# Performance work log

Measured on AMD Instinct MI355X. Metric: run time of the kernel, lower is better.

Reference implementation:

```python
import jax, jax.numpy as jnp
import numpy as np

D_MODEL = 1024
NUM_HEADS = 16
HEAD_DIM = 64
INNER = NUM_HEADS * HEAD_DIM


def setup_inputs() -> dict:
    key = jax.random.key(0)
    k_x, k_q, k_k, k_v, k_o = jax.random.split(key, 5)
    B, T = 4, 2048
    s = 1.0 / np.sqrt(D_MODEL)
    return {
        "x": jax.random.normal(k_x, (B, T, D_MODEL), dtype=jnp.float32),
        "W_q": jax.random.uniform(k_q, (D_MODEL, INNER), dtype=jnp.float32, minval=-s, maxval=s),
        "W_k": jax.random.uniform(k_k, (D_MODEL, INNER), dtype=jnp.float32, minval=-s, maxval=s),
        "W_v": jax.random.uniform(k_v, (D_MODEL, INNER), dtype=jnp.float32, minval=-s, maxval=s),
        "W_o": jax.random.uniform(k_o, (INNER, D_MODEL), dtype=jnp.float32, minval=-s, maxval=s),
    }


def reference(x, W_q, W_k, W_v, W_o):
    B, T, _ = x.shape
    scale = HEAD_DIM ** -0.5
    # project and split heads: [B, H, T, Dh]
    q = (x @ W_q).reshape(B, T, NUM_HEADS, HEAD_DIM).transpose(0, 2, 1, 3)
    k = (x @ W_k).reshape(B, T, NUM_HEADS, HEAD_DIM).transpose(0, 2, 1, 3)
    v = (x @ W_v).reshape(B, T, NUM_HEADS, HEAD_DIM).transpose(0, 2, 1, 3)
    scores = jnp.einsum("bhqd,bhkd->bhqk", q, k) * scale  # [B,H,T,T]
    causal = jnp.tril(jnp.ones((T, T), dtype=bool))
    scores = jnp.where(causal, scores, -jnp.inf)
    probs = jax.nn.softmax(scores, axis=-1)
    ctx = jnp.einsum("bhqk,bhkd->bhqd", probs, v)
    ctx = ctx.transpose(0, 2, 1, 3).reshape(B, T, INNER)
    return ctx @ W_o
```

## Files before the change

### kernel.cpp

```cpp
#include <hip/hip_runtime.h>


typedef short  short8  __attribute__((ext_vector_type(8)));
typedef short  short4v __attribute__((ext_vector_type(4)));
typedef float  floatx4 __attribute__((ext_vector_type(4)));
typedef unsigned uint2v __attribute__((ext_vector_type(2)));

#define T_SZ 2048
#define DM   1024

#define QSCALE 0.18033688011112042f

__device__ __forceinline__ short f2bf(float f) {
  unsigned u = __float_as_uint(f);
  u += 0x7fffu + ((u >> 16) & 1u);
  return (short)(u >> 16);
}

#if defined(__has_builtin) && __has_builtin(__builtin_amdgcn_cvt_pk_bf16_f32)
typedef __bf16 bf16x2_t __attribute__((ext_vector_type(2)));
__device__ __forceinline__ unsigned pack_bf(float lo, float hi) {
  return __builtin_bit_cast(unsigned, __builtin_amdgcn_cvt_pk_bf16_f32(lo, hi));
}
#else
__device__ __forceinline__ unsigned pack_bf(float lo, float hi) {
  return __builtin_amdgcn_perm(__float_as_uint(hi) + 0x8000u,
                               __float_as_uint(lo) + 0x8000u, 0x07060302u);
}
#endif

#if defined(__has_builtin) && __has_builtin(__builtin_amdgcn_exp2f)
__device__ __forceinline__ float fexp2(float x) { return __builtin_amdgcn_exp2f(x); }
#else
__device__ __forceinline__ float fexp2(float x) { return exp2f(x); }
#endif

__device__ __forceinline__ void gll16(const void* g, void* l) {
  __builtin_amdgcn_global_load_lds((const __attribute__((address_space(1))) void*)g,
                                   (__attribute__((address_space(3))) void*)l, 16, 0, 0);
}

#define SBAR() asm volatile("s_barrier" ::: "memory")
#define WLG()  asm volatile("s_waitcnt lgkmcnt(0)" ::: "memory")
#define WV6()  asm volatile("s_waitcnt vmcnt(6)" ::: "memory")
#define WV0()  asm volatile("s_waitcnt vmcnt(0)" ::: "memory")

__global__ void cvt_kernel(const float* __restrict__ s0, const float* __restrict__ s1,
                           const float* __restrict__ s2, const float* __restrict__ s3,
                           short* __restrict__ dst,
                           const float* __restrict__ x, short* __restrict__ xb) {
  const int tx = threadIdx.x, ty = threadIdx.y;
  if (blockIdx.z == 4) {
    const int tid = ty * 32 + tx;
    const int blk = blockIdx.y * 32 + blockIdx.x;
    int i = (blk * 256 + tid) * 4;
#pragma unroll
    for (int j = 0; j < 8; ++j) {
      const float4 v = *(const float4*)(x + i);
      short4v o;
      o.x = f2bf(v.x); o.y = f2bf(v.y); o.z = f2bf(v.z); o.w = f2bf(v.w);
      *(short4v*)(xb + i) = o;
      i += 1048576;
    }
    return;
  }
  const float* srcs[4] = {s0, s1, s2, s3};
  const float* src = srcs[blockIdx.z];
  short* d = dst + (size_t)blockIdx.z * 1048576;
  __shared__ float tile[32][33];
  const int n_base = blockIdx.x * 32, k_base = blockIdx.y * 32;
#pragma unroll
  for (int j = 0; j < 4; ++j)
    tile[ty + j * 8][tx] = src[(size_t)(k_base + ty + j * 8) * 1024 + n_base + tx];
  __syncthreads();
#pragma unroll
  for (int j = 0; j < 4; ++j)
    d[(size_t)(n_base + ty + j * 8) * 1024 + k_base + tx] = f2bf(tile[tx][ty + j * 8]);
}

template <int MODE>
__global__ __launch_bounds__(512, 2) void gemm8(
    const short* __restrict__ A, const short* __restrict__ B,
    short* __restrict__ obf, short* __restrict__ vt, float* __restrict__ of) {
  __shared__ short As[2 * 128 * 64];
  __shared__ short Bs[2 * 256 * 64];
  const int tid  = threadIdx.x;
  const int w    = tid >> 6, lane = tid & 63;
  const int quad = lane >> 4, l15 = lane & 15;
  const int wr   = w >> 2, wc = w & 3;
  const int fx   = l15 & 7;
  const int lid  = (int)blockIdx.x;
  const int xcd  = lid & 7, idx = lid >> 3;
  const int m0   = (idx >> 2) * 128;
  const int n0   = (xcd * 4 + (idx & 3)) * 256;
  const int srow = tid >> 3;
  const int scol = ((tid & 7) ^ (srow & 7)) * 8;

  const short* Ag = A + (size_t)(m0 + srow) * 1024 + scol;
  const short* Bg = B + (size_t)(n0 + srow) * 1024 + scol;

  floatx4 acc[4][4] = {};
  short8 af[4][2], bf[4][2];

#define STG_A(slot, kb) do { \
    short* _lb = &As[(slot) * 8192 + tid * 8]; \
    const short* _gp = Ag + (kb); \
    gll16(_gp, _lb); \
    gll16(_gp + (size_t)(64 * 1024), _lb + 4096); \
  } while (0)
#define STG_B(slot, kb) do { \
    short* _lb = &Bs[(slot) * 16384 + tid * 8]; \
    const short* _gp = Bg + (kb); \
    gll16(_gp,                         _lb); \
    gll16(_gp + (size_t)( 64 * 1024), _lb + 4096); \
    gll16(_gp + (size_t)(128 * 1024), _lb + 8192); \
    gll16(_gp + (size_t)(192 * 1024), _lb + 12288); \
  } while (0)
#define LDA_ALL(slot) do { \
    _Pragma("unroll") for (int ii = 0; ii < 4; ++ii) \
    _Pragma("unroll") for (int s = 0; s < 2; ++s) \
      af[ii][s] = *(const short8*)&As[(slot) * 8192 + \
          (wr * 64 + ii * 16 + l15) * 64 + ((s * 4 + quad) ^ fx) * 8]; \
  } while (0)
#define LDB_ALL(slot) do { \
    _Pragma("unroll") for (int j = 0; j < 4; ++j) \
    _Pragma("unroll") for (int s = 0; s < 2; ++s) \
      bf[j][s] = *(const short8*)&Bs[(slot) * 16384 + \
          (wc * 64 + j * 16 + l15) * 64 + ((s * 4 + quad) ^ fx) * 8]; \
  } while (0)
#define MMH(ih) do { \
    __builtin_amdgcn_s_setprio(1); \
    _Pragma("unroll") for (int i2 = 0; i2 < 2; ++i2) \
    _Pragma("unroll") for (int j = 0; j < 4; ++j) \
    _Pragma("unroll") for (int s = 0; s < 2; ++s) \
      acc[(ih) * 2 + i2][j] = __builtin_amdgcn_mfma_f32_16x16x32_bf16( \
          af[(ih) * 2 + i2][s], bf[j][s], acc[(ih) * 2 + i2][j], 0, 0, 0); \
    __builtin_amdgcn_s_setprio(0); \
  } while (0)

  STG_B(0, 0);  STG_A(0, 0);
  STG_B(1, 64); STG_A(1, 64);
  WV6(); SBAR();

  for (int t = 0; t < 8; ++t) {
    const int kn2 = (2 * t + 2) * 64;
    const int kn3 = (2 * t + 3) * 64;
    const bool mre = (t < 7);
    LDA_ALL(0); LDB_ALL(0);
    SBAR(); WLG();
    MMH(0);
    SBAR();
    if (mre) STG_B(0, kn2);
    if (mre) STG_A(0, kn2);
    MMH(1);
    if (mre) WV6(); else WV0();
    SBAR();
    LDA_ALL(1); LDB_ALL(1);
    SBAR(); WLG();
    MMH(0);
    SBAR();
    if (mre) STG_B(1, kn3);
    if (mre) STG_A(1, kn3);
    MMH(1);
    if (mre) WV6();
    SBAR();
  }

  if constexpr (MODE == 0) {
    const int wsel = m0 >> 10;
    const int nn0  = (m0 & 1023) + wr * 64;
    if (wsel < 2) {
      const float scale = (wsel == 0) ? QSCALE : 1.0f;
      short* outw = obf + (size_t)wsel * (64u * 2048u * 64u);
#pragma unroll
      for (int i = 0; i < 4; ++i) {
        const int nn = nn0 + i * 16 + quad * 4;
        const int h = nn >> 6, d = nn & 63;
#pragma unroll
        for (int j = 0; j < 4; ++j) {
          const int tg = n0 + wc * 64 + j * 16 + l15;
          const int b = tg >> 11, tt = tg & 2047;
          short4v o4;
#pragma unroll
          for (int r = 0; r < 4; ++r) o4[r] = f2bf(acc[i][j][r] * scale);
          *(short4v*)(outw + (((size_t)(b * 16 + h) * 2048 + tt) << 6) + d) = o4;
        }
      }
    } else {
#pragma unroll
      for (int i = 0; i < 4; ++i) {
        const int nn = nn0 + i * 16 + quad * 4;
        const int h = nn >> 6, d = nn & 63;
#pragma unroll
        for (int j = 0; j < 4; ++j) {
          const int tg = n0 + wc * 64 + j * 16 + l15;
          const int b = tg >> 11, tt = tg & 2047;
#pragma unroll
          for (int r = 0; r < 4; ++r)
            vt[(((size_t)(b * 16 + h) * 64 + d + r) << 11) + tt] = f2bf(acc[i][j][r]);
        }
      }
    }
  } else {
    const int nn0 = m0 + wr * 64;
#pragma unroll
    for (int i = 0; i < 4; ++i) {
      const int nn = nn0 + i * 16 + quad * 4;
#pragma unroll
      for (int j = 0; j < 4; ++j) {
        const int tg = n0 + wc * 64 + j * 16 + l15;
        float4 o4;
        o4.x = acc[i][j][0]; o4.y = acc[i][j][1];
        o4.z = acc[i][j][2]; o4.w = acc[i][j][3];
        *(float4*)(of + (size_t)tg * 1024 + nn) = o4;
      }
    }
  }
#undef STG_A
#undef STG_B
#undef LDA_ALL
#undef LDB_ALL
#undef MMH
}

__global__ __launch_bounds__(512, 4) void attn_kernel(
    const short* __restrict__ Qg, const short* __restrict__ Kg,
    const short* __restrict__ Vt, short* __restrict__ ctx) {
  __shared__ short Ks[128 * 72];
  __shared__ short Vs[80 * 136];
  __shared__ short Ps[8 * 32 * 40];

  const int tid  = threadIdx.x;
  const int w    = tid >> 6, lane = tid & 63;
  const int quad = lane >> 4, l15 = lane & 15;
  const int bh = (int)blockIdx.x + 8 * ((int)blockIdx.y & 7);
  const int g  = (int)blockIdx.y >> 3;
  const int qb = (g < 4) ? (7 - g) : (g - 4);
  const int b  = bh >> 4, h = bh & 15;

  const size_t base = (size_t)bh * (T_SZ * 64);
  const short* Qb  = Qg + base;
  const short* Kb  = Kg + base;
  const short* Vtb = Vt + base;
  short* Pw = &Ps[w * 1280];

  const int skr = tid >> 2, skp = (tid & 3) * 16;
  const int svr = tid >> 3, svp = (tid & 7) * 16;

  if (tid < 256) {
    const int rr = 64 + (tid >> 4), cb = (tid & 15) * 8;
    const short vv = (tid < 16) ? (short)0x3F80 : (short)0;
    short8 fill;
#pragma unroll
    for (int j = 0; j < 8; ++j) fill[j] = vv;
    *(short8*)&Vs[rr * 136 + cb] = fill;
  }

  const int rowA = qb * 256 + w * 32;
  const int rowB = rowA + 16;
  const int ktmax = 2 * qb + 2;

  const short8 qA0 = *(const short8*)(Qb + (size_t)(rowA + l15) * 64 + quad * 8);
  const short8 qA1 = *(const short8*)(Qb + (size_t)(rowA + l15) * 64 + 32 + quad * 8);
  const short8 qB0 = *(const short8*)(Qb + (size_t)(rowB + l15) * 64 + quad * 8);
  const short8 qB1 = *(const short8*)(Qb + (size_t)(rowB + l15) * 64 + 32 + quad * 8);

  floatx4 OA[4] = {}, OB[4] = {};
  floatx4 O5A = {}, O5B = {};

  short8 kR[2], vR[2];
  kR[0] = *(const short8*)(Kb + (size_t)skr * 64 + skp);
  kR[1] = *(const short8*)(Kb + (size_t)skr * 64 + skp + 8);
  vR[0] = *(const short8*)(Vtb + (size_t)svr * 2048 + svp);
  vR[1] = *(const short8*)(Vtb + (size_t)svr * 2048 + svp + 8);

  for (int kt = 0; kt < ktmax; ++kt) {
    const int k0 = kt << 7;
    __syncthreads();
    *(short8*)&Ks[skr * 72 + skp]     = kR[0];
    *(short8*)&Ks[skr * 72 + skp + 8] = kR[1];
    *(short8*)&Vs[svr * 136 + svp]     = vR[0];
    *(short8*)&Vs[svr * 136 + svp + 8] = vR[1];
    if (kt + 1 < ktmax) {
      const int kn = (kt + 1) << 7;
      kR[0] = *(const short8*)(Kb + (size_t)(kn + skr) * 64 + skp);
      kR[1] = *(const short8*)(Kb + (size_t)(kn + skr) * 64 + skp + 8);
      vR[0] = *(const short8*)(Vtb + (size_t)svr * 2048 + kn + svp);
      vR[1] = *(const short8*)(Vtb + (size_t)svr * 2048 + kn + svp + 8);
    }
    __syncthreads();

    const int dkA = rowA - k0;
    if (dkA < 0) continue;
    const int dkB = dkA + 16;
    const int limA = dkA + l15, limB = limA + 16;
    const int naA = min(8, (dkA >> 4) + 1), nchA = (naA + 1) >> 1;
    const int naB = min(8, (dkB >> 4) + 1), nchB = (naB + 1) >> 1;

#pragma unroll
    for (int c = 0; c < 4; ++c) {
      if (c < nchB) {
#pragma unroll
        for (int mm = 0; mm < 2; ++mm) {
          const int mt = 2 * c + mm;
          const int pa = l15 * 40 + mm * 16 + quad * 4;
          const int pb = (16 + l15) * 40 + mm * 16 + quad * 4;
          const bool aB = (mt * 16 < dkB + 16);
          const bool aA = (mt * 16 < dkA + 16);
          if (aB) {
            const short8 kf0 = *(const short8*)&Ks[(mt * 16 + l15) * 72 + quad * 8];
            const short8 kf1 = *(const short8*)&Ks[(mt * 16 + l15) * 72 + 32 + quad * 8];
            {
              floatx4 s = {};
              s = __builtin_amdgcn_mfma_f32_16x16x32_bf16(kf0, qB0, s, 0, 0, 0);
              s = __builtin_amdgcn_mfma_f32_16x16x32_bf16(kf1, qB1, s, 0, 0, 0);
              if (mt * 16 + 15 > dkB) {
#pragma unroll
                for (int r = 0; r < 4; ++r)
                  if (mt * 16 + quad * 4 + r > limB) s[r] = -1e30f;
              }
              floatx4 e;
#pragma unroll
              for (int r = 0; r < 4; ++r) e[r] = fexp2(s[r]);
              uint2v pd;
              pd.x = pack_bf(e[0], e[1]);
              pd.y = pack_bf(e[2], e[3]);
              *(uint2v*)&Pw[pb] = pd;
            }
            if (c < nchA) {
              if (aA) {
                floatx4 s = {};
                s = __builtin_amdgcn_mfma_f32_16x16x32_bf16(kf0, qA0, s, 0, 0, 0);
                s = __builtin_amdgcn_mfma_f32_16x16x32_bf16(kf1, qA1, s, 0, 0, 0);
                if (mt * 16 + 15 > dkA) {
#pragma unroll
                  for (int r = 0; r < 4; ++r)
                    if (mt * 16 + quad * 4 + r > limA) s[r] = -1e30f;
                }
                floatx4 e;
#pragma unroll
                for (int r = 0; r < 4; ++r) e[r] = fexp2(s[r]);
                uint2v pd;
                pd.x = pack_bf(e[0], e[1]);
                pd.y = pack_bf(e[2], e[3]);
                *(uint2v*)&Pw[pa] = pd;
              } else {
                uint2v z; z.x = 0; z.y = 0;
                *(uint2v*)&Pw[pa] = z;
              }
            }
          } else {
            uint2v z; z.x = 0; z.y = 0;
            *(uint2v*)&Pw[pb] = z;
            if (c < nchA) *(uint2v*)&Pw[pa] = z;
          }
        }
        const int vcol = c * 32 + quad * 8;
        const short8 vfl = *(const short8*)&Vs[(64 + l15) * 136 + vcol];
        short8 vf[4];
#pragma unroll
        for (int dt = 0; dt < 4; ++dt)
          vf[dt] = *(const short8*)&Vs[(dt * 16 + l15) * 136 + vcol];
        const short8 pfB = *(const short8*)&Pw[(16 + l15) * 40 + quad * 8];
#pragma unroll
        for (int dt = 0; dt < 4; ++dt)
          OB[dt] = __builtin_amdgcn_mfma_f32_16x16x32_bf16(vf[dt], pfB, OB[dt], 0, 0, 0);
        O5B = __builtin_amdgcn_mfma_f32_16x16x32_bf16(vfl, pfB, O5B, 0, 0, 0);
        if (c < nchA) {
          const short8 pfA = *(const short8*)&Pw[l15 * 40 + quad * 8];
#pragma unroll
          for (int dt = 0; dt < 4; ++dt)
            OA[dt] = __builtin_amdgcn_mfma_f32_16x16x32_bf16(vf[dt], pfA, OA[dt], 0, 0, 0);
          O5A = __builtin_amdgcn_mfma_f32_16x16x32_bf16(vfl, pfA, O5A, 0, 0, 0);
        }
      }
    }
  }

  {
    const float lA = __shfl(O5A[0], l15);
    const float invA = 1.0f / lA;
    const int t = rowA + l15;
    short* cb = ctx + (((size_t)(b * T_SZ + t)) << 10) + h * 64 + quad * 4;
#pragma unroll
    for (int dt = 0; dt < 4; ++dt) {
      short4v o4;
#pragma unroll
      for (int r = 0; r < 4; ++r) o4[r] = f2bf(OA[dt][r] * invA);
      *(short4v*)(cb + dt * 16) = o4;
    }
  }
  {
    const float lB = __shfl(O5B[0], l15);
    const float invB = 1.0f / lB;
    const int t = rowB + l15;
    short* cb = ctx + (((size_t)(b * T_SZ + t)) << 10) + h * 64 + quad * 4;
#pragma unroll
    for (int dt = 0; dt < 4; ++dt) {
      short4v o4;
#pragma unroll
      for (int r = 0; r < 4; ++r) o4[r] = f2bf(OB[dt][r] * invB);
      *(short4v*)(cb + dt * 16) = o4;
    }
  }
}

extern "C" void kernel_launch(void* const* d_in, const int* in_sizes, int n_in,
                              void* d_out, int out_size, void* d_ws, size_t ws_size,
                              hipStream_t stream) {
  const float* x  = (const float*)d_in[0];
  const float* Wq = (const float*)d_in[1];
  const float* Wk = (const float*)d_in[2];
  const float* Wv = (const float*)d_in[3];
  const float* Wo = (const float*)d_in[4];
  float* out = (float*)d_out;

  short* ws  = (short*)d_ws;
  short* xb  = ws;
  short* Wt  = ws + 8388608;
  short* Qb  = Wt + 4 * 1048576;
  short* Kb  = Qb + 8388608;
  short* Vt  = Kb + 8388608;
  short* ctx = xb;

  cvt_kernel<<<dim3(32, 32, 5), dim3(32, 8), 0, stream>>>(Wq, Wk, Wv, Wo, Wt, x, xb);
  gemm8<0><<<dim3(768), 512, 0, stream>>>(Wt, xb, Qb, Vt, nullptr);
  attn_kernel<<<dim3(8, 64), 512, 0, stream>>>(Qb, Kb, Vt, ctx);
  gemm8<1><<<dim3(256), 512, 0, stream>>>(Wt + 3 * 1048576, ctx, nullptr, nullptr, out);
}
```

Baseline: 236.7 us.

## Shrink GEMM tile to 128x128 with 4 waves and finer-grained staging

```diff
diff --git a/kernel.cpp b/kernel.cpp
--- a/kernel.cpp
+++ b/kernel.cpp
@@ -42,7 +42,7 @@
 
 #define SBAR() asm volatile("s_barrier" ::: "memory")
 #define WLG()  asm volatile("s_waitcnt lgkmcnt(0)" ::: "memory")
-#define WV6()  asm volatile("s_waitcnt vmcnt(6)" ::: "memory")
+#define WV8()  asm volatile("s_waitcnt vmcnt(8)" ::: "memory")
 #define WV0()  asm volatile("s_waitcnt vmcnt(0)" ::: "memory")
 
 __global__ void cvt_kernel(const float* __restrict__ s0, const float* __restrict__ s1,
@@ -79,20 +79,20 @@
 }
 
 template <int MODE>
-__global__ __launch_bounds__(512, 2) void gemm8(
+__global__ __launch_bounds__(256, 2) void gemm4(
     const short* __restrict__ A, const short* __restrict__ B,
     short* __restrict__ obf, short* __restrict__ vt, float* __restrict__ of) {
   __shared__ short As[2 * 128 * 64];
-  __shared__ short Bs[2 * 256 * 64];
+  __shared__ short Bs[2 * 128 * 64];
   const int tid  = threadIdx.x;
   const int w    = tid >> 6, lane = tid & 63;
   const int quad = lane >> 4, l15 = lane & 15;
-  const int wr   = w >> 2, wc = w & 3;
+  const int wr   = w >> 1, wc = w & 1;
   const int fx   = l15 & 7;
   const int lid  = (int)blockIdx.x;
   const int xcd  = lid & 7, idx = lid >> 3;
-  const int m0   = (idx >> 2) * 128;
-  const int n0   = (xcd * 4 + (idx & 3)) * 256;
+  const int m0   = (idx >> 3) * 128;
+  const int n0   = (xcd * 8 + (idx & 7)) * 128;
   const int srow = tid >> 3;
   const int scol = ((tid & 7) ^ (srow & 7)) * 8;
 
@@ -100,69 +100,75 @@
   const short* Bg = B + (size_t)(n0 + srow) * 1024 + scol;
 
   floatx4 acc[4][4] = {};
-  short8 af[4][2], bf[4][2];
-
-#define STG_A(slot, kb) do { \
-    short* _lb = &As[(slot) * 8192 + tid * 8]; \
-    const short* _gp = Ag + (kb); \
-    gll16(_gp, _lb); \
-    gll16(_gp + (size_t)(64 * 1024), _lb + 4096); \
-  } while (0)
-#define STG_B(slot, kb) do { \
-    short* _lb = &Bs[(slot) * 16384 + tid * 8]; \
-    const short* _gp = Bg + (kb); \
-    gll16(_gp,                         _lb); \
-    gll16(_gp + (size_t)( 64 * 1024), _lb + 4096); \
-    gll16(_gp + (size_t)(128 * 1024), _lb + 8192); \
-    gll16(_gp + (size_t)(192 * 1024), _lb + 12288); \
-  } while (0)
-#define LDA_ALL(slot) do { \
-    _Pragma("unroll") for (int ii = 0; ii < 4; ++ii) \
+  short8 af[2][2], bf[4][2];
+
+#define SA0(slot, kb) do { \
+    gll16(Ag + (kb),                        &As[(slot) * 8192 + tid * 8]); \
+    gll16(Ag + (size_t)(32 * 1024) + (kb),  &As[(slot) * 8192 + 2048 + tid * 8]); \
+  } while (0)
+#define SA1(slot, kb) do { \
+    gll16(Ag + (size_t)(64 * 1024) + (kb),  &As[(slot) * 8192 + 4096 + tid * 8]); \
+    gll16(Ag + (size_t)(96 * 1024) + (kb),  &As[(slot) * 8192 + 6144 + tid * 8]); \
+  } while (0)
+#define SB0(slot, kb) do { \
+    gll16(Bg + (kb),                        &Bs[(slot) * 8192 + tid * 8]); \
+    gll16(Bg + (size_t)(32 * 1024) + (kb),  &Bs[(slot) * 8192 + 2048 + tid * 8]); \
+  } while (0)
+#define SB1(slot, kb) do { \
+    gll16(Bg + (size_t)(64 * 1024) + (kb),  &Bs[(slot) * 8192 + 4096 + tid * 8]); \
+    gll16(Bg + (size_t)(96 * 1024) + (kb),  &Bs[(slot) * 8192 + 6144 + tid * 8]); \
+  } while (0)
+#define LDA4(slot, ih) do { \
+    _Pragma("unroll") for (int ii = 0; ii < 2; ++ii) \
     _Pragma("unroll") for (int s = 0; s < 2; ++s) \
       af[ii][s] = *(const short8*)&As[(slot) * 8192 + \
-          (wr * 64 + ii * 16 + l15) * 64 + ((s * 4 + quad) ^ fx) * 8]; \
-  } while (0)
-#define LDB_ALL(slot) do { \
+          (wr * 64 + (ih) * 32 + ii * 16 + l15) * 64 + ((s * 4 + quad) ^ fx) * 8]; \
+  } while (0)
+#define LDB8(slot) do { \
     _Pragma("unroll") for (int j = 0; j < 4; ++j) \
     _Pragma("unroll") for (int s = 0; s < 2; ++s) \
-      bf[j][s] = *(const short8*)&Bs[(slot) * 16384 + \
+      bf[j][s] = *(const short8*)&Bs[(slot) * 8192 + \
           (wc * 64 + j * 16 + l15) * 64 + ((s * 4 + quad) ^ fx) * 8]; \
   } while (0)
-#define MMH(ih) do { \
+#define MMQ(ih, jh) do { \
     __builtin_amdgcn_s_setprio(1); \
-    _Pragma("unroll") for (int i2 = 0; i2 < 2; ++i2) \
-    _Pragma("unroll") for (int j = 0; j < 4; ++j) \
+    _Pragma("unroll") for (int ii = 0; ii < 2; ++ii) \
+    _Pragma("unroll") for (int jj = 0; jj < 2; ++jj) \
     _Pragma("unroll") for (int s = 0; s < 2; ++s) \
-      acc[(ih) * 2 + i2][j] = __builtin_amdgcn_mfma_f32_16x16x32_bf16( \
-          af[(ih) * 2 + i2][s], bf[j][s], acc[(ih) * 2 + i2][j], 0, 0, 0); \
+      acc[(ih) * 2 + ii][(jh) * 2 + jj] = __builtin_amdgcn_mfma_f32_16x16x32_bf16( \
+          af[ii][s], bf[(jh) * 2 + jj][s], acc[(ih) * 2 + ii][(jh) * 2 + jj], 0, 0, 0); \
     __builtin_amdgcn_s_setprio(0); \
   } while (0)
 
-  STG_B(0, 0);  STG_A(0, 0);
-  STG_B(1, 64); STG_A(1, 64);
-  WV6(); SBAR();
+  SB0(0, 0);  SB1(0, 0);  SA0(0, 0);  SA1(0, 0);
+  SB0(1, 64); SB1(1, 64); SA0(1, 64); SA1(1, 64);
+  WV8(); SBAR();
 
   for (int t = 0; t < 8; ++t) {
     const int kn2 = (2 * t + 2) * 64;
     const int kn3 = (2 * t + 3) * 64;
     const bool mre = (t < 7);
-    LDA_ALL(0); LDB_ALL(0);
-    SBAR(); WLG();
-    MMH(0);
+    LDA4(0, 0); LDB8(0);
+    SBAR(); WLG(); MMQ(0, 0); SBAR();
+    if (mre) SB0(0, kn2);
+    MMQ(0, 1); SBAR();
+    LDA4(0, 1);
+    if (mre) SB1(0, kn2);
+    SBAR(); WLG(); MMQ(1, 0); SBAR();
+    if (mre) { SA0(0, kn2); SA1(0, kn2); }
+    MMQ(1, 1);
+    if (mre) WV8(); else WV0();
     SBAR();
-    if (mre) STG_B(0, kn2);
-    if (mre) STG_A(0, kn2);
-    MMH(1);
-    if (mre) WV6(); else WV0();
-    SBAR();
-    LDA_ALL(1); LDB_ALL(1);
-    SBAR(); WLG();
-    MMH(0);
-    SBAR();
-    if (mre) STG_B(1, kn3);
-    if (mre) STG_A(1, kn3);
-    MMH(1);
-    if (mre) WV6();
+    LDA4(1, 0); LDB8(1);
+    SBAR(); WLG(); MMQ(0, 0); SBAR();
+    if (mre) SB0(1, kn3);
+    MMQ(0, 1); SBAR();
+    LDA4(1, 1);
+    if (mre) SB1(1, kn3);
+    SBAR(); WLG(); MMQ(1, 0); SBAR();
+    if (mre) { SA0(1, kn3); SA1(1, kn3); }
+    MMQ(1, 1);
+    if (mre) WV8();
     SBAR();
   }
 
@@ -216,11 +222,13 @@
       }
     }
   }
-#undef STG_A
-#undef STG_B
-#undef LDA_ALL
-#undef LDB_ALL
-#undef MMH
+#undef SA0
+#undef SA1
+#undef SB0
+#undef SB1
+#undef LDA4
+#undef LDB8
+#undef MMQ
 }
 
 __global__ __launch_bounds__(512, 4) void attn_kernel(
@@ -424,7 +432,7 @@
   short* ctx = xb;
 
   cvt_kernel<<<dim3(32, 32, 5), dim3(32, 8), 0, stream>>>(Wq, Wk, Wv, Wo, Wt, x, xb);
-  gemm8<0><<<dim3(768), 512, 0, stream>>>(Wt, xb, Qb, Vt, nullptr);
+  gemm4<0><<<dim3(1536), 256, 0, stream>>>(Wt, xb, Qb, Vt, nullptr);
   attn_kernel<<<dim3(8, 64), 512, 0, stream>>>(Qb, Kb, Vt, ctx);
-  gemm8<1><<<dim3(256), 512, 0, stream>>>(Wt + 3 * 1048576, ctx, nullptr, nullptr, out);
-}
+  gemm4<1><<<dim3(512), 256, 0, stream>>>(Wt + 3 * 1048576, ctx, nullptr, nullptr, out);
+}
```

Result: no change. 240.1 us (+1.4%).

## Double-buffer P tiles in attention and add dedicated pipelined QKV projection GEMM

Applied to the files above, without the earlier changes.

```diff
diff --git a/kernel.cpp b/kernel.cpp
--- a/kernel.cpp
+++ b/kernel.cpp
@@ -76,6 +76,131 @@
 #pragma unroll
   for (int j = 0; j < 4; ++j)
     d[(size_t)(n_base + ty + j * 8) * 1024 + k_base + tx] = f2bf(tile[tx][ty + j * 8]);
+}
+
+__global__ __launch_bounds__(512, 2) void gemm_qkvT(
+    const short* __restrict__ Wt, const short* __restrict__ xb,
+    short* __restrict__ obf, short* __restrict__ vt) {
+  __shared__ short As[2 * 128 * 64];
+  __shared__ short Bs[2 * 256 * 64];
+  const int tid  = threadIdx.x;
+  const int w    = tid >> 6, lane = tid & 63;
+  const int quad = lane >> 4, l15 = lane & 15;
+  const int wr   = w >> 2, wc = w & 3;
+  const int fx   = l15 & 7;
+  const int lid  = (int)blockIdx.x;
+  const int xcd  = lid & 7, idx = lid >> 3;
+  const int m0   = (idx >> 2) * 128;
+  const int n0   = (xcd * 4 + (idx & 3)) * 256;
+  const int srow = tid >> 3;
+  const int scol = ((tid & 7) ^ (srow & 7)) * 8;
+
+  const short* Ag = Wt + (size_t)(m0 + srow) * 1024 + scol;
+  const short* Bg = xb + (size_t)(n0 + srow) * 1024 + scol;
+
+  floatx4 acc[4][4] = {};
+  short8 af[2][2], bf[4][2];
+
+#define STG_A(slot, kb) do { \
+    short* _lb = &As[(slot) * 8192 + tid * 8]; \
+    gll16(Ag + (kb), _lb); \
+    gll16(Ag + (size_t)(64 * 1024) + (kb), _lb + 4096); \
+  } while (0)
+#define STG_B(slot, h, kb) do { \
+    short* _lb = &Bs[(slot) * 16384 + (h) * 8192 + tid * 8]; \
+    const short* _gp = Bg + (size_t)(h) * (128 * 1024) + (kb); \
+    gll16(_gp, _lb); \
+    gll16(_gp + (size_t)(64 * 1024), _lb + 4096); \
+  } while (0)
+#define LDA2(slot, ih) do { \
+    _Pragma("unroll") for (int ii = 0; ii < 2; ++ii) \
+    _Pragma("unroll") for (int s = 0; s < 2; ++s) \
+      af[ii][s] = *(const short8*)&As[(slot) * 8192 + \
+          (wr * 64 + (ih) * 32 + ii * 16 + l15) * 64 + ((s * 4 + quad) ^ fx) * 8]; \
+  } while (0)
+#define LDB8(slot) do { \
+    _Pragma("unroll") for (int j = 0; j < 4; ++j) \
+    _Pragma("unroll") for (int s = 0; s < 2; ++s) \
+      bf[j][s] = *(const short8*)&Bs[(slot) * 16384 + \
+          (wc * 64 + j * 16 + l15) * 64 + ((s * 4 + quad) ^ fx) * 8]; \
+  } while (0)
+#define MMQ(ih, jh) do { \
+    __builtin_amdgcn_s_setprio(1); \
+    _Pragma("unroll") for (int ii = 0; ii < 2; ++ii) \
+    _Pragma("unroll") for (int jj = 0; jj < 2; ++jj) \
+    _Pragma("unroll") for (int s = 0; s < 2; ++s) \
+      acc[(ih) * 2 + ii][(jh) * 2 + jj] = __builtin_amdgcn_mfma_f32_16x16x32_bf16( \
+          af[ii][s], bf[(jh) * 2 + jj][s], acc[(ih) * 2 + ii][(jh) * 2 + jj], 0, 0, 0); \
+    __builtin_amdgcn_s_setprio(0); \
+  } while (0)
+
+  STG_B(0, 0, 0);  STG_B(0, 1, 0);  STG_A(0, 0);
+  STG_B(1, 0, 64); STG_B(1, 1, 64); STG_A(1, 64);
+  WV6(); SBAR();
+
+  for (int t = 0; t < 8; ++t) {
+    const int kn2 = (2 * t + 2) * 64;
+    const int kn3 = (2 * t + 3) * 64;
+    const bool mre = (t < 7);
+    LDA2(0, 0); LDB8(0);
+    SBAR(); WLG(); MMQ(0, 0); SBAR();
+    if (mre) STG_B(0, 0, kn2);
+    SBAR(); MMQ(0, 1); SBAR();
+    LDA2(0, 1);
+    if (mre) STG_B(0, 1, kn2);
+    SBAR(); WLG(); MMQ(1, 0); SBAR();
+    if (mre) { STG_A(0, kn2); WV6(); } else { WV0(); }
+    SBAR(); MMQ(1, 1); SBAR();
+    LDA2(1, 0); LDB8(1);
+    SBAR(); WLG(); MMQ(0, 0); SBAR();
+    if (mre) STG_B(1, 0, kn3);
+    SBAR(); MMQ(0, 1); SBAR();
+    LDA2(1, 1);
+    if (mre) STG_B(1, 1, kn3);
+    SBAR(); WLG(); MMQ(1, 0); SBAR();
+    if (mre) { STG_A(1, kn3); WV6(); }
+    SBAR(); MMQ(1, 1); SBAR();
+  }
+
+  const int wsel = m0 >> 10;
+  const int nn0  = (m0 & 1023) + wr * 64;
+  if (wsel < 2) {
+    const float scale = (wsel == 0) ? QSCALE : 1.0f;
+    short* outw = obf + (size_t)wsel * (64u * 2048u * 64u);
+#pragma unroll
+    for (int i = 0; i < 4; ++i) {
+      const int nn = nn0 + i * 16 + quad * 4;
+      const int h = nn >> 6, d = nn & 63;
+#pragma unroll
+      for (int j = 0; j < 4; ++j) {
+        const int tg = n0 + wc * 64 + j * 16 + l15;
+        const int b = tg >> 11, tt = tg & 2047;
+        short4v o4;
+#pragma unroll
+        for (int r = 0; r < 4; ++r) o4[r] = f2bf(acc[i][j][r] * scale);
+        *(short4v*)(outw + (((size_t)(b * 16 + h) * 2048 + tt) << 6) + d) = o4;
+      }
+    }
+  } else {
+#pragma unroll
+    for (int i = 0; i < 4; ++i) {
+      const int nn = nn0 + i * 16 + quad * 4;
+      const int h = nn >> 6, d = nn & 63;
+#pragma unroll
+      for (int j = 0; j < 4; ++j) {
+        const int tg = n0 + wc * 64 + j * 16 + l15;
+        const int b = tg >> 11, tt = tg & 2047;
+#pragma unroll
+        for (int r = 0; r < 4; ++r)
+          vt[(((size_t)(b * 16 + h) * 64 + d + r) << 11) + tt] = f2bf(acc[i][j][r]);
+      }
+    }
+  }
+#undef STG_A
+#undef STG_B
+#undef LDA2
+#undef LDB8
+#undef MMQ
 }
 
 template <int MODE>
@@ -228,7 +353,7 @@
     const short* __restrict__ Vt, short* __restrict__ ctx) {
   __shared__ short Ks[128 * 72];
   __shared__ short Vs[80 * 136];
-  __shared__ short Ps[8 * 32 * 40];
+  __shared__ short Ps[8 * 2 * 32 * 36];
 
   const int tid  = threadIdx.x;
   const int w    = tid >> 6, lane = tid & 63;
@@ -242,7 +367,7 @@
   const short* Qb  = Qg + base;
   const short* Kb  = Kg + base;
   const short* Vtb = Vt + base;
-  short* Pw = &Ps[w * 1280];
+  short* Pw = &Ps[w * 2304];
 
   const int skr = tid >> 2, skp = (tid & 3) * 16;
   const int svr = tid >> 3, svp = (tid & 7) * 16;
@@ -297,27 +422,43 @@
     const int naA = min(8, (dkA >> 4) + 1), nchA = (naA + 1) >> 1;
     const int naB = min(8, (dkB >> 4) + 1), nchB = (naB + 1) >> 1;
 
-#pragma unroll
-    for (int c = 0; c < 4; ++c) {
-      if (c < nchB) {
-#pragma unroll
-        for (int mm = 0; mm < 2; ++mm) {
-          const int mt = 2 * c + mm;
-          const int pa = l15 * 40 + mm * 16 + quad * 4;
-          const int pb = (16 + l15) * 40 + mm * 16 + quad * 4;
-          const bool aB = (mt * 16 < dkB + 16);
-          const bool aA = (mt * 16 < dkA + 16);
-          if (aB) {
-            const short8 kf0 = *(const short8*)&Ks[(mt * 16 + l15) * 72 + quad * 8];
-            const short8 kf1 = *(const short8*)&Ks[(mt * 16 + l15) * 72 + 32 + quad * 8];
-            {
+    auto QKT = [&](int c, int pb0) {
+#pragma unroll
+      for (int mm = 0; mm < 2; ++mm) {
+        const int mt = 2 * c + mm;
+        const int pa = pb0 + l15 * 36 + mm * 16 + quad * 4;
+        const int pb = pb0 + (16 + l15) * 36 + mm * 16 + quad * 4;
+        const bool aB = (mt * 16 < dkB + 16);
+        const bool aA = (mt * 16 < dkA + 16);
+        if (aB) {
+          const short8 kf0 = *(const short8*)&Ks[(mt * 16 + l15) * 72 + quad * 8];
+          const short8 kf1 = *(const short8*)&Ks[(mt * 16 + l15) * 72 + 32 + quad * 8];
+          {
+            floatx4 s = {};
+            s = __builtin_amdgcn_mfma_f32_16x16x32_bf16(kf0, qB0, s, 0, 0, 0);
+            s = __builtin_amdgcn_mfma_f32_16x16x32_bf16(kf1, qB1, s, 0, 0, 0);
+            if (mt * 16 + 15 > dkB) {
+#pragma unroll
+              for (int r = 0; r < 4; ++r)
+                if (mt * 16 + quad * 4 + r > limB) s[r] = -1e30f;
+            }
+            floatx4 e;
+#pragma unroll
+            for (int r = 0; r < 4; ++r) e[r] = fexp2(s[r]);
+            uint2v pd;
+            pd.x = pack_bf(e[0], e[1]);
+            pd.y = pack_bf(e[2], e[3]);
+            *(uint2v*)&Pw[pb] = pd;
+          }
+          if (c < nchA) {
+            if (aA) {
               floatx4 s = {};
-              s = __builtin_amdgcn_mfma_f32_16x16x32_bf16(kf0, qB0, s, 0, 0, 0);
-              s = __builtin_amdgcn_mfma_f32_16x16x32_bf16(kf1, qB1, s, 0, 0, 0);
-              if (mt * 16 + 15 > dkB) {
+              s = __builtin_amdgcn_mfma_f32_16x16x32_bf16(kf0, qA0, s, 0, 0, 0);
+              s = __builtin_amdgcn_mfma_f32_16x16x32_bf16(kf1, qA1, s, 0, 0, 0);
+              if (mt * 16 + 15 > dkA) {
 #pragma unroll
                 for (int r = 0; r < 4; ++r)
-                  if (mt * 16 + quad * 4 + r > limB) s[r] = -1e30f;
+                  if (mt * 16 + quad * 4 + r > limA) s[r] = -1e30f;
               }
               floatx4 e;
 #pragma unroll
@@ -325,54 +466,49 @@
               uint2v pd;
               pd.x = pack_bf(e[0], e[1]);
               pd.y = pack_bf(e[2], e[3]);
-              *(uint2v*)&Pw[pb] = pd;
+              *(uint2v*)&Pw[pa] = pd;
+            } else {
+              uint2v z; z.x = 0; z.y = 0;
+              *(uint2v*)&Pw[pa] = z;
             }
-            if (c < nchA) {
-              if (aA) {
-                floatx4 s = {};
-                s = __builtin_amdgcn_mfma_f32_16x16x32_bf16(kf0, qA0, s, 0, 0, 0);
-                s = __builtin_amdgcn_mfma_f32_16x16x32_bf16(kf1, qA1, s, 0, 0, 0);
-                if (mt * 16 + 15 > dkA) {
-#pragma unroll
-                  for (int r = 0; r < 4; ++r)
-                    if (mt * 16 + quad * 4 + r > limA) s[r] = -1e30f;
-                }
-                floatx4 e;
-#pragma unroll
-                for (int r = 0; r < 4; ++r) e[r] = fexp2(s[r]);
-                uint2v pd;
-                pd.x = pack_bf(e[0], e[1]);
-                pd.y = pack_bf(e[2], e[3]);
-                *(uint2v*)&Pw[pa] = pd;
-              } else {
-                uint2v z; z.x = 0; z.y = 0;
-                *(uint2v*)&Pw[pa] = z;
-              }
-            }
-          } else {
-            uint2v z; z.x = 0; z.y = 0;
-            *(uint2v*)&Pw[pb] = z;
-            if (c < nchA) *(uint2v*)&Pw[pa] = z;
           }
+        } else {
+          uint2v z; z.x = 0; z.y = 0;
+          *(uint2v*)&Pw[pb] = z;
+          if (c < nchA) *(uint2v*)&Pw[pa] = z;
         }
-        const int vcol = c * 32 + quad * 8;
-        const short8 vfl = *(const short8*)&Vs[(64 + l15) * 136 + vcol];
-        short8 vf[4];
+      }
+    };
+
+    auto PV = [&](int c, int pb0) {
+      const int vcol = c * 32 + quad * 8;
+      const short8 vfl = *(const short8*)&Vs[(64 + l15) * 136 + vcol];
+      short8 vf[4];
+#pragma unroll
+      for (int dt = 0; dt < 4; ++dt)
+        vf[dt] = *(const short8*)&Vs[(dt * 16 + l15) * 136 + vcol];
+      const short8 pfB = *(const short8*)&Pw[pb0 + (16 + l15) * 36 + quad * 8];
+      __builtin_amdgcn_s_setprio(1);
+#pragma unroll
+      for (int dt = 0; dt < 4; ++dt)
+        OB[dt] = __builtin_amdgcn_mfma_f32_16x16x32_bf16(vf[dt], pfB, OB[dt], 0, 0, 0);
+      O5B = __builtin_amdgcn_mfma_f32_16x16x32_bf16(vfl, pfB, O5B, 0, 0, 0);
+      if (c < nchA) {
+        const short8 pfA = *(const short8*)&Pw[pb0 + l15 * 36 + quad * 8];
 #pragma unroll
         for (int dt = 0; dt < 4; ++dt)
-          vf[dt] = *(const short8*)&Vs[(dt * 16 + l15) * 136 + vcol];
-        const short8 pfB = *(const short8*)&Pw[(16 + l15) * 40 + quad * 8];
-#pragma unroll
-        for (int dt = 0; dt < 4; ++dt)
-          OB[dt] = __builtin_amdgcn_mfma_f32_16x16x32_bf16(vf[dt], pfB, OB[dt], 0, 0, 0);
-        O5B = __builtin_amdgcn_mfma_f32_16x16x32_bf16(vfl, pfB, O5B, 0, 0, 0);
-        if (c < nchA) {
-          const short8 pfA = *(const short8*)&Pw[l15 * 40 + quad * 8];
-#pragma unroll
-          for (int dt = 0; dt < 4; ++dt)
-            OA[dt] = __builtin_amdgcn_mfma_f32_16x16x32_bf16(vf[dt], pfA, OA[dt], 0, 0, 0);
-          O5A = __builtin_amdgcn_mfma_f32_16x16x32_bf16(vfl, pfA, O5A, 0, 0, 0);
-        }
+          OA[dt] = __builtin_amdgcn_mfma_f32_16x16x32_bf16(vf[dt], pfA, OA[dt], 0, 0, 0);
+        O5A = __builtin_amdgcn_mfma_f32_16x16x32_bf16(vfl, pfA, O5A, 0, 0, 0);
+      }
+      __builtin_amdgcn_s_setprio(0);
+    };
+
+    QKT(0, 0);
+#pragma unroll
+    for (int c = 0; c < 4; ++c) {
+      if (c < nchB) {
+        if (c + 1 < nchB) QKT(c + 1, ((c + 1) & 1) * 1152);
+        PV(c, (c & 1) * 1152);
       }
     }
   }
@@ -424,7 +560,7 @@
   short* ctx = xb;
 
   cvt_kernel<<<dim3(32, 32, 5), dim3(32, 8), 0, stream>>>(Wq, Wk, Wv, Wo, Wt, x, xb);
-  gemm8<0><<<dim3(768), 512, 0, stream>>>(Wt, xb, Qb, Vt, nullptr);
+  gemm_qkvT<<<dim3(768), 512, 0, stream>>>(Wt, xb, Qb, Vt);
   attn_kernel<<<dim3(8, 64), 512, 0, stream>>>(Qb, Kb, Vt, ctx);
   gemm8<1><<<dim3(256), 512, 0, stream>>>(Wt + 3 * 1048576, ctx, nullptr, nullptr, out);
 }
```

Result: slower. 252.0 us (+6.5%).

## Fuse Q/K/V projections into one persistent GEMM reusing x tile across weights

Applied to the files above, without the earlier changes.

```diff
diff --git a/kernel.cpp b/kernel.cpp
--- a/kernel.cpp
+++ b/kernel.cpp
@@ -78,10 +78,144 @@
     d[(size_t)(n_base + ty + j * 8) * 1024 + k_base + tx] = f2bf(tile[tx][ty + j * 8]);
 }
 
-template <int MODE>
-__global__ __launch_bounds__(512, 2) void gemm8(
+__global__ __launch_bounds__(512, 2) void gemm_qkv3(
+    const short* __restrict__ Wt, const short* __restrict__ xb,
+    short* __restrict__ obf, short* __restrict__ vt) {
+  __shared__ short As[2 * 128 * 64];
+  __shared__ short Bs[2 * 256 * 64];
+  const int tid  = threadIdx.x;
+  const int w    = tid >> 6, lane = tid & 63;
+  const int quad = lane >> 4, l15 = lane & 15;
+  const int wr   = w >> 2, wc = w & 3;
+  const int fx   = l15 & 7;
+  const int lid  = (int)blockIdx.x;
+  const int xcd  = lid & 7, idx = lid >> 3;
+  const int m_base = (idx >> 2) * 128;
+  const int n0   = (xcd * 4 + (idx & 3)) * 256;
+  const int srow = tid >> 3;
+  const int scol = ((tid & 7) ^ (srow & 7)) * 8;
+
+  const short* Ag = Wt + (size_t)(m_base + srow) * 1024 + scol;
+  const short* Bg = xb + (size_t)(n0 + srow) * 1024 + scol;
+
+  floatx4 acc[4][4] = {};
+  short8 af[4][2], bf[4][2];
+
+#define STG_A(slot, kb, base) do { \
+    short* _lb = &As[(slot) * 8192 + tid * 8]; \
+    const short* _gp = (base) + (kb); \
+    gll16(_gp, _lb); \
+    gll16(_gp + (size_t)(64 * 1024), _lb + 4096); \
+  } while (0)
+#define STG_B(slot, kb) do { \
+    short* _lb = &Bs[(slot) * 16384 + tid * 8]; \
+    const short* _gp = Bg + (kb); \
+    gll16(_gp,                         _lb); \
+    gll16(_gp + (size_t)( 64 * 1024), _lb + 4096); \
+    gll16(_gp + (size_t)(128 * 1024), _lb + 8192); \
+    gll16(_gp + (size_t)(192 * 1024), _lb + 12288); \
+  } while (0)
+#define LDA_ALL(slot) do { \
+    _Pragma("unroll") for (int ii = 0; ii < 4; ++ii) \
+    _Pragma("unroll") for (int s = 0; s < 2; ++s) \
+      af[ii][s] = *(const short8*)&As[(slot) * 8192 + \
+          (wr * 64 + ii * 16 + l15) * 64 + ((s * 4 + quad) ^ fx) * 8]; \
+  } while (0)
+#define LDB_ALL(slot) do { \
+    _Pragma("unroll") for (int j = 0; j < 4; ++j) \
+    _Pragma("unroll") for (int s = 0; s < 2; ++s) \
+      bf[j][s] = *(const short8*)&Bs[(slot) * 16384 + \
+          (wc * 64 + j * 16 + l15) * 64 + ((s * 4 + quad) ^ fx) * 8]; \
+  } while (0)
+#define MMH(ih) do { \
+    __builtin_amdgcn_s_setprio(1); \
+    _Pragma("unroll") for (int i2 = 0; i2 < 2; ++i2) \
+    _Pragma("unroll") for (int j = 0; j < 4; ++j) \
+    _Pragma("unroll") for (int s = 0; s < 2; ++s) \
+      acc[(ih) * 2 + i2][j] = __builtin_amdgcn_mfma_f32_16x16x32_bf16( \
+          af[(ih) * 2 + i2][s], bf[j][s], acc[(ih) * 2 + i2][j], 0, 0, 0); \
+    __builtin_amdgcn_s_setprio(0); \
+  } while (0)
+
+  STG_B(0, 0);  STG_A(0, 0, Ag);
+  STG_B(1, 64); STG_A(1, 64, Ag);
+  WV6(); SBAR();
+
+  for (int rep = 0; rep < 3; ++rep) {
+    const int nn0 = m_base + wr * 64;
+    for (int t = 0; t < 8; ++t) {
+      const bool wrap = (t == 7);
+      const bool last = (rep == 2) && wrap;
+      const short* Asrc = wrap ? (Ag + 1048576) : Ag;
+      const int kb2 = wrap ? 0  : (2 * t + 2) * 64;
+      const int kb3 = wrap ? 64 : (2 * t + 3) * 64;
+      LDA_ALL(0); LDB_ALL(0);
+      SBAR(); WLG();
+      MMH(0);
+      SBAR();
+      if (!last) { STG_B(0, kb2); STG_A(0, kb2, Asrc); }
+      MMH(1);
+      if (!last) WV6(); else WV0();
+      SBAR();
+      LDA_ALL(1); LDB_ALL(1);
+      SBAR(); WLG();
+      MMH(0);
+      SBAR();
+      if (!last) { STG_B(1, kb3); STG_A(1, kb3, Asrc); }
+      MMH(1);
+      if (wrap) {
+        if (rep < 2) {
+          const float scale = (rep == 0) ? QSCALE : 1.0f;
+          short* outw = obf + (size_t)rep * (64u * 2048u * 64u);
+#pragma unroll
+          for (int i = 0; i < 4; ++i) {
+            const int nn = nn0 + i * 16 + quad * 4;
+            const int h = nn >> 6, d = nn & 63;
+#pragma unroll
+            for (int j = 0; j < 4; ++j) {
+              const int tg = n0 + wc * 64 + j * 16 + l15;
+              const int b = tg >> 11, tt = tg & 2047;
+              short4v o4;
+#pragma unroll
+              for (int r = 0; r < 4; ++r) o4[r] = f2bf(acc[i][j][r] * scale);
+              *(short4v*)(outw + (((size_t)(b * 16 + h) * 2048 + tt) << 6) + d) = o4;
+            }
+          }
+        } else {
+#pragma unroll
+          for (int i = 0; i < 4; ++i) {
+            const int nn = nn0 + i * 16 + quad * 4;
+            const int h = nn >> 6, d = nn & 63;
+#pragma unroll
+            for (int j = 0; j < 4; ++j) {
+              const int tg = n0 + wc * 64 + j * 16 + l15;
+              const int b = tg >> 11, tt = tg & 2047;
+#pragma unroll
+              for (int r = 0; r < 4; ++r)
+                vt[(((size_t)(b * 16 + h) * 64 + d + r) << 11) + tt] = f2bf(acc[i][j][r]);
+            }
+          }
+        }
+#pragma unroll
+        for (int i = 0; i < 4; ++i)
+#pragma unroll
+          for (int j = 0; j < 4; ++j) acc[i][j] = (floatx4){0.f, 0.f, 0.f, 0.f};
+      }
+      if (!last) WV6();
+      SBAR();
+    }
+    Ag += 1048576;
+  }
+#undef STG_A
+#undef STG_B
+#undef LDA_ALL
+#undef LDB_ALL
+#undef MMH
+}
+
+__global__ __launch_bounds__(512, 2) void gemm8W(
     const short* __restrict__ A, const short* __restrict__ B,
-    short* __restrict__ obf, short* __restrict__ vt, float* __restrict__ of) {
+    float* __restrict__ of) {
   __shared__ short As[2 * 128 * 64];
   __shared__ short Bs[2 * 256 * 64];
   const int tid  = threadIdx.x;
@@ -166,54 +300,17 @@
     SBAR();
   }
 
-  if constexpr (MODE == 0) {
-    const int wsel = m0 >> 10;
-    const int nn0  = (m0 & 1023) + wr * 64;
-    if (wsel < 2) {
-      const float scale = (wsel == 0) ? QSCALE : 1.0f;
-      short* outw = obf + (size_t)wsel * (64u * 2048u * 64u);
-#pragma unroll
-      for (int i = 0; i < 4; ++i) {
-        const int nn = nn0 + i * 16 + quad * 4;
-        const int h = nn >> 6, d = nn & 63;
-#pragma unroll
-        for (int j = 0; j < 4; ++j) {
-          const int tg = n0 + wc * 64 + j * 16 + l15;
-          const int b = tg >> 11, tt = tg & 2047;
-          short4v o4;
-#pragma unroll
-          for (int r = 0; r < 4; ++r) o4[r] = f2bf(acc[i][j][r] * scale);
-          *(short4v*)(outw + (((size_t)(b * 16 + h) * 2048 + tt) << 6) + d) = o4;
-        }
-      }
-    } else {
-#pragma unroll
-      for (int i = 0; i < 4; ++i) {
-        const int nn = nn0 + i * 16 + quad * 4;
-        const int h = nn >> 6, d = nn & 63;
-#pragma unroll
-        for (int j = 0; j < 4; ++j) {
-          const int tg = n0 + wc * 64 + j * 16 + l15;
-          const int b = tg >> 11, tt = tg & 2047;
-#pragma unroll
-          for (int r = 0; r < 4; ++r)
-            vt[(((size_t)(b * 16 + h) * 64 + d + r) << 11) + tt] = f2bf(acc[i][j][r]);
-        }
-      }
-    }
-  } else {
-    const int nn0 = m0 + wr * 64;
-#pragma unroll
-    for (int i = 0; i < 4; ++i) {
-      const int nn = nn0 + i * 16 + quad * 4;
-#pragma unroll
-      for (int j = 0; j < 4; ++j) {
-        const int tg = n0 + wc * 64 + j * 16 + l15;
-        float4 o4;
-        o4.x = acc[i][j][0]; o4.y = acc[i][j][1];
-        o4.z = acc[i][j][2]; o4.w = acc[i][j][3];
-        *(float4*)(of + (size_t)tg * 1024 + nn) = o4;
-      }
+  const int nn0 = m0 + wr * 64;
+#pragma unroll
+  for (int i = 0; i < 4; ++i) {
+    const int nn = nn0 + i * 16 + quad * 4;
+#pragma unroll
+    for (int j = 0; j < 4; ++j) {
+      const int tg = n0 + wc * 64 + j * 16 + l15;
+      float4 o4;
+      o4.x = acc[i][j][0]; o4.y = acc[i][j][1];
+      o4.z = acc[i][j][2]; o4.w = acc[i][j][3];
+      *(float4*)(of + (size_t)tg * 1024 + nn) = o4;
     }
   }
 #undef STG_A
@@ -227,7 +324,7 @@
     const short* __restrict__ Qg, const short* __restrict__ Kg,
     const short* __restrict__ Vt, short* __restrict__ ctx) {
   __shared__ short Ks[128 * 72];
-  __shared__ short Vs[80 * 136];
+  __shared__ short Vs[64 * 136];
   __shared__ short Ps[8 * 32 * 40];
 
   const int tid  = threadIdx.x;
@@ -247,13 +344,11 @@
   const int skr = tid >> 2, skp = (tid & 3) * 16;
   const int svr = tid >> 3, svp = (tid & 7) * 16;
 
-  if (tid < 256) {
-    const int rr = 64 + (tid >> 4), cb = (tid & 15) * 8;
-    const short vv = (tid < 16) ? (short)0x3F80 : (short)0;
-    short8 fill;
-#pragma unroll
-    for (int j = 0; j < 8; ++j) fill[j] = vv;
-    *(short8*)&Vs[rr * 136 + cb] = fill;
+  short8 vfl_c;
+  {
+    const short vv = (l15 == 0) ? (short)0x3F80 : (short)0;
+#pragma unroll
+    for (int j = 0; j < 8; ++j) vfl_c[j] = vv;
   }
 
   const int rowA = qb * 256 + w * 32;
@@ -356,7 +451,6 @@
           }
         }
         const int vcol = c * 32 + quad * 8;
-        const short8 vfl = *(const short8*)&Vs[(64 + l15) * 136 + vcol];
         short8 vf[4];
 #pragma unroll
         for (int dt = 0; dt < 4; ++dt)
@@ -365,13 +459,13 @@
 #pragma unroll
         for (int dt = 0; dt < 4; ++dt)
           OB[dt] = __builtin_amdgcn_mfma_f32_16x16x32_bf16(vf[dt], pfB, OB[dt], 0, 0, 0);
-        O5B = __builtin_amdgcn_mfma_f32_16x16x32_bf16(vfl, pfB, O5B, 0, 0, 0);
+        O5B = __builtin_amdgcn_mfma_f32_16x16x32_bf16(vfl_c, pfB, O5B, 0, 0, 0);
         if (c < nchA) {
           const short8 pfA = *(const short8*)&Pw[l15 * 40 + quad * 8];
 #pragma unroll
           for (int dt = 0; dt < 4; ++dt)
             OA[dt] = __builtin_amdgcn_mfma_f32_16x16x32_bf16(vf[dt], pfA, OA[dt], 0, 0, 0);
-          O5A = __builtin_amdgcn_mfma_f32_16x16x32_bf16(vfl, pfA, O5A, 0, 0, 0);
+          O5A = __builtin_amdgcn_mfma_f32_16x16x32_bf16(vfl_c, pfA, O5A, 0, 0, 0);
         }
       }
     }
@@ -424,7 +518,7 @@
   short* ctx = xb;
 
   cvt_kernel<<<dim3(32, 32, 5), dim3(32, 8), 0, stream>>>(Wq, Wk, Wv, Wo, Wt, x, xb);
-  gemm8<0><<<dim3(768), 512, 0, stream>>>(Wt, xb, Qb, Vt, nullptr);
+  gemm_qkv3<<<dim3(256), 512, 0, stream>>>(Wt, xb, Qb, Vt);
   attn_kernel<<<dim3(8, 64), 512, 0, stream>>>(Qb, Kb, Vt, ctx);
-  gemm8<1><<<dim3(256), 512, 0, stream>>>(Wt + 3 * 1048576, ctx, nullptr, nullptr, out);
-}
+  gemm8W<<<dim3(256), 512, 0, stream>>>(Wt + 3 * 1048576, ctx, out);
+}
```

After: 245.1 us. +3.6%, slower.
